# Kernel optimization log

Measured on AMD Instinct MI355X. Metric: run time of the kernel, lower is better.

The kernel has to match this reference:

```python
import jax, jax.numpy as jnp
import numpy as np

DIST_THRESHOLD = 900.0  # distance_threshold from __init__
NO_CODE_ID = -1         # no_code_id from __init__


def setup_inputs() -> dict:
    key = jax.random.key(0)
    k1, k2 = jax.random.split(key)
    x = jax.random.normal(k1, (4, 2048, 512), dtype=jnp.float32)      # [b, n, d] tokens
    codes = jax.random.normal(k2, (16384, 512), dtype=jnp.float32)    # [c, d] full codebook
    return {"x": x, "codes": codes}


def reference(x, codes):
    x2 = jnp.sum(x * x, axis=-1, keepdims=True)            # [b, n, 1]
    c2 = jnp.sum(codes * codes, axis=-1)                   # [c]
    xc = jnp.einsum('bnd,cd->bnc', x, codes)               # [b, n, c] (the compute-heavy GEMM)
    dist_sq = jnp.maximum(x2 + c2 - 2.0 * xc, 0.0)         # clamp tiny negatives, like cdist

    within = jnp.any(dist_sq <= DIST_THRESHOLD, axis=-1)   # [b, n]
    nn_ids = jnp.argmin(dist_sq, axis=-1)                  # [b, n]
    ids = jnp.where(within, nn_ids, NO_CODE_ID)            # tokens outside threshold -> no_code_id
    return ids
```

## Files before the change

### kernel.cpp

```cpp
#include <hip/hip_runtime.h>


#define NTOK   8192
#define NCODES 16384
#define DDIM   512
#define NCHUNK 8
#define CHUNK  2048
#define DIST_THR 900.0f

typedef unsigned short u16;
typedef _Float16 half8 __attribute__((ext_vector_type(8)));
typedef float    f32x4 __attribute__((ext_vector_type(4)));

__global__ __launch_bounds__(256) void nn_conv(const float* __restrict__ src,
                                               u16* __restrict__ dh,
                                               u16* __restrict__ dl) {
    int c = blockIdx.x * 256 + threadIdx.x;
    int r = c & 15, q = (c >> 4) & 3, g = (c >> 6) & 7, kit = (c >> 9) & 15;
    int tile = c >> 13;
    int row = tile * 128 + g * 16 + r;
    int k = kit * 32 + q * 8;
    const float* p = src + (size_t)row * DDIM + k;
    float4 v0 = *(const float4*)p;
    float4 v1 = *(const float4*)(p + 4);
    float vv[8] = {v0.x, v0.y, v0.z, v0.w, v1.x, v1.y, v1.z, v1.w};
    u16 hs[8], ls[8];
    #pragma unroll
    for (int j = 0; j < 8; ++j) {
        float sv = vv[j] * 16.0f;
        _Float16 h = (_Float16)sv;
        float hf = (float)h;
        _Float16 l = (_Float16)(sv - hf);
        union { _Float16 f; u16 u; } uh, ul;
        uh.f = h; ul.f = l;
        hs[j] = uh.u; ls[j] = ul.u;
    }
    uint4 H, L;
    H.x = hs[0] | ((unsigned)hs[1] << 16); H.y = hs[2] | ((unsigned)hs[3] << 16);
    H.z = hs[4] | ((unsigned)hs[5] << 16); H.w = hs[6] | ((unsigned)hs[7] << 16);
    L.x = ls[0] | ((unsigned)ls[1] << 16); L.y = ls[2] | ((unsigned)ls[3] << 16);
    L.z = ls[4] | ((unsigned)ls[5] << 16); L.w = ls[6] | ((unsigned)ls[7] << 16);
    *(uint4*)(dh + (size_t)c * 8) = H;
    *(uint4*)(dl + (size_t)c * 8) = L;
}

__global__ __launch_bounds__(256) void nn_c2(const float* __restrict__ codes,
                                             float* __restrict__ c2) {
    int w = threadIdx.x >> 6;
    int lane = threadIdx.x & 63;
    int c = blockIdx.x * 4 + w;
    const float* p = codes + (size_t)c * DDIM + lane * 8;
    float4 v0 = *(const float4*)p;
    float4 v1 = *(const float4*)(p + 4);
    float s = v0.x*v0.x + v0.y*v0.y + v0.z*v0.z + v0.w*v0.w
            + v1.x*v1.x + v1.y*v1.y + v1.z*v1.z + v1.w*v1.w;
    #pragma unroll
    for (int off = 32; off > 0; off >>= 1) s += __shfl_down(s, off);
    if (lane == 0) c2[c] = s;
}

#define SM_C2 33024
__global__ __launch_bounds__(256) void nn_gemm(const u16* __restrict__ xh,
                                               const u16* __restrict__ xl,
                                               const u16* __restrict__ chh,
                                               const u16* __restrict__ cll,
                                               const float* __restrict__ c2,
                                               float* __restrict__ pmin,
                                               int* __restrict__ pid) {
    __shared__ __align__(16) char smem[SM_C2 + CHUNK * 4];
    const int tid = threadIdx.x;
    const int lane = tid & 63;
    const int wave = tid >> 6;
    const int wm = wave & 1;
    const int wn = wave >> 1;
    const int mtile = blockIdx.x >> 3;
    const int chunk = blockIdx.x & 7;
    const int m0 = mtile * 128;

    for (int i = tid; i < CHUNK; i += 256)
        *(float*)(smem + SM_C2 + i * 4) = c2[chunk * CHUNK + i];

    float mv[16];
    int   mi[16];
    #pragma unroll
    for (int s = 0; s < 16; ++s) { mv[s] = 3.4e38f; mi[s] = 0; }

    for (int nt = 0; nt < 16; ++nt) {
        f32x4 acc[4][4];
        #pragma unroll
        for (int i = 0; i < 4; ++i)
            #pragma unroll
            for (int j = 0; j < 4; ++j) acc[i][j] = (f32x4)0.0f;

        for (int kit = 0; kit < 16; ++kit) {
            const u16* gsrc;
            if (wave < 2) {
                size_t off = ((size_t)(mtile * 16 + kit)) * 4096;
                gsrc = (wave == 0 ? xh : xl) + off;
            } else {
                size_t off = ((size_t)((chunk * 16 + nt) * 16 + kit)) * 4096;
                gsrc = (wave == 2 ? chh : cll) + off;
            }
            char* ldsbase = smem + wave * 8192;
            #pragma unroll
            for (int jj = 0; jj < 8; ++jj) {
                __builtin_amdgcn_global_load_lds(
                    (const __attribute__((address_space(1))) void*)(gsrc + jj * 512 + lane * 8),
                    (__attribute__((address_space(3))) void*)(ldsbase + jj * 1024),
                    16, 0, 0);
            }
            __syncthreads();

            const char* Ah = smem;
            const char* Al = smem + 8192;
            const char* Bh = smem + 16384;
            const char* Bl = smem + 24576;
            half8 ah[4], al[4];
            #pragma unroll
            for (int i = 0; i < 4; ++i) {
                int g = wm * 4 + i;
                ah[i] = *(const half8*)(Ah + g * 1024 + lane * 16);
                al[i] = *(const half8*)(Al + g * 1024 + lane * 16);
            }
            #pragma unroll
            for (int j = 0; j < 4; ++j) {
                int g = wn * 4 + j;
                half8 bh = *(const half8*)(Bh + g * 1024 + lane * 16);
                half8 bl = *(const half8*)(Bl + g * 1024 + lane * 16);
                #pragma unroll
                for (int i = 0; i < 4; ++i) {
                    acc[i][j] = __builtin_amdgcn_mfma_f32_16x16x32_f16(ah[i], bh, acc[i][j], 0, 0, 0);
                    acc[i][j] = __builtin_amdgcn_mfma_f32_16x16x32_f16(ah[i], bl, acc[i][j], 0, 0, 0);
                    acc[i][j] = __builtin_amdgcn_mfma_f32_16x16x32_f16(al[i], bh, acc[i][j], 0, 0, 0);
                }
            }
            __syncthreads();
        }

        #pragma unroll
        for (int j = 0; j < 4; ++j) {
            int ncol = nt * 128 + wn * 64 + j * 16 + (lane & 15);
            float cv = *(const float*)(smem + SM_C2 + ncol * 4);
            int gid = chunk * CHUNK + ncol;
            #pragma unroll
            for (int i = 0; i < 4; ++i)
                #pragma unroll
                for (int r = 0; r < 4; ++r) {
                    float s = fmaf(acc[i][j][r], -0.0078125f, cv);
                    int slot = i * 4 + r;
                    if (s < mv[slot]) { mv[slot] = s; mi[slot] = gid; }
                }
        }
    }

    {
        int contrib = wn * 16 + (lane & 15);
        #pragma unroll
        for (int i = 0; i < 4; ++i)
            #pragma unroll
            for (int r = 0; r < 4; ++r) {
                int row = wm * 64 + i * 16 + ((lane >> 4) & 3) * 4 + r;
                int2 e;
                e.x = __float_as_int(mv[i * 4 + r]);
                e.y = mi[i * 4 + r];
                *(int2*)(smem + contrib * 1032 + row * 8) = e;
            }
    }
    __syncthreads();
    if (tid < 128) {
        int2 e = *(const int2*)(smem + tid * 8);
        float bv = __int_as_float(e.x);
        int bi = e.y;
        for (int k = 1; k < 32; ++k) {
            int2 t2 = *(const int2*)(smem + k * 1032 + tid * 8);
            float v = __int_as_float(t2.x);
            if (v < bv || (v == bv && t2.y < bi)) { bv = v; bi = t2.y; }
        }
        pmin[(size_t)(m0 + tid) * NCHUNK + chunk] = bv;
        pid [(size_t)(m0 + tid) * NCHUNK + chunk] = bi;
    }
}

__global__ __launch_bounds__(256) void nn_fin(const float* __restrict__ x,
                                              const float* __restrict__ pmin,
                                              const int* __restrict__ pid,
                                              int* __restrict__ out) {
    int w = threadIdx.x >> 6;
    int lane = threadIdx.x & 63;
    int t = blockIdx.x * 4 + w;
    const float* p = x + (size_t)t * DDIM + lane * 8;
    float4 v0 = *(const float4*)p;
    float4 v1 = *(const float4*)(p + 4);
    float s = v0.x*v0.x + v0.y*v0.y + v0.z*v0.z + v0.w*v0.w
            + v1.x*v1.x + v1.y*v1.y + v1.z*v1.z + v1.w*v1.w;
    #pragma unroll
    for (int off = 32; off > 0; off >>= 1) s += __shfl_down(s, off);
    if (lane == 0) {
        const float* pm = pmin + (size_t)t * NCHUNK;
        const int*   pi = pid  + (size_t)t * NCHUNK;
        float bv = pm[0]; int bi = pi[0];
        #pragma unroll
        for (int c = 1; c < NCHUNK; ++c) {
            float v = pm[c]; int id = pi[c];
            if (v < bv || (v == bv && id < bi)) { bv = v; bi = id; }
        }
        float mind = s + bv;
        out[t] = (mind <= DIST_THR) ? bi : -1;
    }
}

extern "C" void kernel_launch(void* const* d_in, const int* in_sizes, int n_in,
                              void* d_out, int out_size, void* d_ws, size_t ws_size,
                              hipStream_t stream) {
    const float* x     = (const float*)d_in[0];
    const float* codes = (const float*)d_in[1];
    int* out = (int*)d_out;

    char* ws = (char*)d_ws;
    u16*   xh   = (u16*)(ws);
    u16*   xl   = (u16*)(ws + 8388608);
    u16*   chh  = (u16*)(ws + 16777216);
    u16*   cll  = (u16*)(ws + 33554432);
    float* c2   = (float*)(ws + 50331648);
    float* pmin = (float*)(ws + 50397184);
    int*   pid  = (int*)  (ws + 50659328);

    nn_conv<<<NTOK   * 64 / 256, 256, 0, stream>>>(x, xh, xl);
    nn_conv<<<NCODES * 64 / 256, 256, 0, stream>>>(codes, chh, cll);
    nn_c2<<<NCODES / 4, 256, 0, stream>>>(codes, c2);
    nn_gemm<<<64 * NCHUNK, 256, 0, stream>>>(xh, xl, chh, cll, c2, pmin, pid);
    nn_fin<<<NTOK / 4, 256, 0, stream>>>(x, pmin, pid, out);
}
```

Baseline: 461.2 us.

## Split codebook into 16 chunks, fuse prep kernels, shuffle-reduce argmin

```diff
diff --git a/kernel.cpp b/kernel.cpp
--- a/kernel.cpp
+++ b/kernel.cpp
@@ -4,18 +4,17 @@
 #define NTOK   8192
 #define NCODES 16384
 #define DDIM   512
-#define NCHUNK 8
-#define CHUNK  2048
+#define NCHUNK 16
+#define CHUNK  1024
 #define DIST_THR 900.0f
 
 typedef unsigned short u16;
 typedef _Float16 half8 __attribute__((ext_vector_type(8)));
 typedef float    f32x4 __attribute__((ext_vector_type(4)));
 
-__global__ __launch_bounds__(256) void nn_conv(const float* __restrict__ src,
-                                               u16* __restrict__ dh,
-                                               u16* __restrict__ dl) {
-    int c = blockIdx.x * 256 + threadIdx.x;
+__device__ __forceinline__ void conv_body(const float* __restrict__ src,
+                                          u16* __restrict__ dh,
+                                          u16* __restrict__ dl, int c) {
     int r = c & 15, q = (c >> 4) & 3, g = (c >> 6) & 7, kit = (c >> 9) & 15;
     int tile = c >> 13;
     int row = tile * 128 + g * 16 + r;
@@ -44,48 +43,54 @@
     *(uint4*)(dl + (size_t)c * 8) = L;
 }
 
-__global__ __launch_bounds__(256) void nn_c2(const float* __restrict__ codes,
-                                             float* __restrict__ c2) {
-    int w = threadIdx.x >> 6;
-    int lane = threadIdx.x & 63;
-    int c = blockIdx.x * 4 + w;
-    const float* p = codes + (size_t)c * DDIM + lane * 8;
-    float4 v0 = *(const float4*)p;
-    float4 v1 = *(const float4*)(p + 4);
-    float s = v0.x*v0.x + v0.y*v0.y + v0.z*v0.z + v0.w*v0.w
-            + v1.x*v1.x + v1.y*v1.y + v1.z*v1.z + v1.w*v1.w;
-    #pragma unroll
-    for (int off = 32; off > 0; off >>= 1) s += __shfl_down(s, off);
-    if (lane == 0) c2[c] = s;
-}
-
-#define SM_C2 33024
-__global__ __launch_bounds__(256) void nn_gemm(const u16* __restrict__ xh,
-                                               const u16* __restrict__ xl,
-                                               const u16* __restrict__ chh,
-                                               const u16* __restrict__ cll,
-                                               const float* __restrict__ c2,
-                                               float* __restrict__ pmin,
-                                               int* __restrict__ pid) {
-    __shared__ __align__(16) char smem[SM_C2 + CHUNK * 4];
+__global__ __launch_bounds__(256) void nn_prep(const float* __restrict__ x,
+                                               const float* __restrict__ codes,
+                                               u16* __restrict__ xh, u16* __restrict__ xl,
+                                               u16* __restrict__ ch, u16* __restrict__ cl,
+                                               float* __restrict__ c2) {
+    int b = blockIdx.x;
+    if (b < 2048) {
+        conv_body(x, xh, xl, b * 256 + threadIdx.x);
+    } else if (b < 6144) {
+        conv_body(codes, ch, cl, (b - 2048) * 256 + threadIdx.x);
+    } else {
+        int w = threadIdx.x >> 6;
+        int lane = threadIdx.x & 63;
+        int c = (b - 6144) * 4 + w;
+        const float* p = codes + (size_t)c * DDIM + lane * 8;
+        float4 v0 = *(const float4*)p;
+        float4 v1 = *(const float4*)(p + 4);
+        float s = v0.x*v0.x + v0.y*v0.y + v0.z*v0.z + v0.w*v0.w
+                + v1.x*v1.x + v1.y*v1.y + v1.z*v1.z + v1.w*v1.w;
+        #pragma unroll
+        for (int off = 32; off > 0; off >>= 1) s += __shfl_down(s, off);
+        if (lane == 0) c2[c] = s;
+    }
+}
+
+__global__ __launch_bounds__(256, 4) void nn_gemm(const u16* __restrict__ xh,
+                                                  const u16* __restrict__ xl,
+                                                  const u16* __restrict__ chh,
+                                                  const u16* __restrict__ cll,
+                                                  const float* __restrict__ c2,
+                                                  float* __restrict__ pmin,
+                                                  int* __restrict__ pid) {
+    __shared__ __align__(16) char smem[32768];
     const int tid = threadIdx.x;
     const int lane = tid & 63;
     const int wave = tid >> 6;
     const int wm = wave & 1;
     const int wn = wave >> 1;
-    const int mtile = blockIdx.x >> 3;
-    const int chunk = blockIdx.x & 7;
+    const int mtile = blockIdx.x >> 4;
+    const int chunk = blockIdx.x & 15;
     const int m0 = mtile * 128;
-
-    for (int i = tid; i < CHUNK; i += 256)
-        *(float*)(smem + SM_C2 + i * 4) = c2[chunk * CHUNK + i];
 
     float mv[16];
     int   mi[16];
     #pragma unroll
     for (int s = 0; s < 16; ++s) { mv[s] = 3.4e38f; mi[s] = 0; }
 
-    for (int nt = 0; nt < 16; ++nt) {
+    for (int nt = 0; nt < 8; ++nt) {
         f32x4 acc[4][4];
         #pragma unroll
         for (int i = 0; i < 4; ++i)
@@ -98,7 +103,7 @@
                 size_t off = ((size_t)(mtile * 16 + kit)) * 4096;
                 gsrc = (wave == 0 ? xh : xl) + off;
             } else {
-                size_t off = ((size_t)((chunk * 16 + nt) * 16 + kit)) * 4096;
+                size_t off = ((size_t)((chunk * 8 + nt) * 16 + kit)) * 4096;
                 gsrc = (wave == 2 ? chh : cll) + off;
             }
             char* ldsbase = smem + wave * 8192;
@@ -140,8 +145,8 @@
         #pragma unroll
         for (int j = 0; j < 4; ++j) {
             int ncol = nt * 128 + wn * 64 + j * 16 + (lane & 15);
-            float cv = *(const float*)(smem + SM_C2 + ncol * 4);
             int gid = chunk * CHUNK + ncol;
+            float cv = c2[gid];
             #pragma unroll
             for (int i = 0; i < 4; ++i)
                 #pragma unroll
@@ -153,29 +158,34 @@
         }
     }
 
-    {
-        int contrib = wn * 16 + (lane & 15);
+    #pragma unroll
+    for (int off = 1; off < 16; off <<= 1) {
+        #pragma unroll
+        for (int s = 0; s < 16; ++s) {
+            float ov = __shfl_xor(mv[s], off);
+            int   oi = __shfl_xor(mi[s], off);
+            if (ov < mv[s] || (ov == mv[s] && oi < mi[s])) { mv[s] = ov; mi[s] = oi; }
+        }
+    }
+    if ((lane & 15) == 0) {
         #pragma unroll
         for (int i = 0; i < 4; ++i)
             #pragma unroll
             for (int r = 0; r < 4; ++r) {
-                int row = wm * 64 + i * 16 + ((lane >> 4) & 3) * 4 + r;
+                int row = wm * 64 + i * 16 + (lane >> 4) * 4 + r;
                 int2 e;
                 e.x = __float_as_int(mv[i * 4 + r]);
                 e.y = mi[i * 4 + r];
-                *(int2*)(smem + contrib * 1032 + row * 8) = e;
+                *(int2*)(smem + (wn * 128 + row) * 8) = e;
             }
     }
     __syncthreads();
     if (tid < 128) {
-        int2 e = *(const int2*)(smem + tid * 8);
-        float bv = __int_as_float(e.x);
-        int bi = e.y;
-        for (int k = 1; k < 32; ++k) {
-            int2 t2 = *(const int2*)(smem + k * 1032 + tid * 8);
-            float v = __int_as_float(t2.x);
-            if (v < bv || (v == bv && t2.y < bi)) { bv = v; bi = t2.y; }
-        }
+        int2 e0 = *(const int2*)(smem + tid * 8);
+        int2 e1 = *(const int2*)(smem + (128 + tid) * 8);
+        float v0 = __int_as_float(e0.x), v1 = __int_as_float(e1.x);
+        float bv = v0; int bi = e0.y;
+        if (v1 < bv || (v1 == bv && e1.y < bi)) { bv = v1; bi = e1.y; }
         pmin[(size_t)(m0 + tid) * NCHUNK + chunk] = bv;
         pid [(size_t)(m0 + tid) * NCHUNK + chunk] = bi;
     }
@@ -223,11 +233,9 @@
     u16*   cll  = (u16*)(ws + 33554432);
     float* c2   = (float*)(ws + 50331648);
     float* pmin = (float*)(ws + 50397184);
-    int*   pid  = (int*)  (ws + 50659328);
-
-    nn_conv<<<NTOK   * 64 / 256, 256, 0, stream>>>(x, xh, xl);
-    nn_conv<<<NCODES * 64 / 256, 256, 0, stream>>>(codes, chh, cll);
-    nn_c2<<<NCODES / 4, 256, 0, stream>>>(codes, c2);
+    int*   pid  = (int*)  (ws + 50921472);
+
+    nn_prep<<<10240, 256, 0, stream>>>(x, codes, xh, xl, chh, cll, c2);
     nn_gemm<<<64 * NCHUNK, 256, 0, stream>>>(xh, xl, chh, cll, c2, pmin, pid);
     nn_fin<<<NTOK / 4, 256, 0, stream>>>(x, pmin, pid, out);
 }
```

Result: no change. 462.2 us (+0.2%).
